# Kernel tuning notes

Measured on AMD Instinct MI355X. Metric: run time of the kernel, lower is better.

Reference implementation:

```python
import jax, jax.numpy as jnp
import numpy as np

VERY_NEGATIVE_NUMBER = -1e30


def setup_inputs() -> dict:
    key = jax.random.key(0)
    ks = jax.random.split(key, 7)
    B, N, M, D = 16, 1024, 1024, 128
    inv_sqrt_d = 1.0 / np.sqrt(D).astype(np.float32)
    query = jax.random.normal(ks[0], (B, N, D), jnp.float32)
    memory = jax.random.normal(ks[1], (B, M, D), jnp.float32)
    # trilinear similarity parameters (BiDAF)
    w_q = jax.random.normal(ks[2], (D,), jnp.float32) * inv_sqrt_d
    w_m = jax.random.normal(ks[3], (D,), jnp.float32) * inv_sqrt_d
    w_qm = jax.random.normal(ks[4], (D,), jnp.float32) * inv_sqrt_d
    query_mask = jax.random.randint(ks[5], (B, N), 0, 2, jnp.int32)
    memory_mask = jax.random.randint(ks[6], (B, M), 0, 2, jnp.int32)
    return {
        "query": query,
        "memory": memory,
        "w_q": w_q,
        "w_m": w_m,
        "w_qm": w_qm,
        "query_mask": query_mask,
        "memory_mask": memory_mask,
    }


def reference(query, memory, w_q, w_m, w_qm, query_mask, memory_mask):
    # trilinear similarity: sim[b,n,m] = w_q.q_n + w_m.m_m + sum_d w_qm_d * q_nd * m_md
    sim = (
        jnp.einsum("bnd,d->bn", query, w_q)[:, :, None]
        + jnp.einsum("bmd,d->bm", memory, w_m)[:, None, :]
        + jnp.einsum("bnd,d,bmd->bnm", query, w_qm, memory)
    )  # [B, N, M]
    mask = (
        query_mask[:, :, None].astype(sim.dtype)
        * memory_mask[:, None, :].astype(sim.dtype)
    )  # [B, N, M]
    sim = sim + (1.0 - mask) * VERY_NEGATIVE_NUMBER
    # query -> memory attention (row-wise softmax over memory axis)
    q2m_prob = jax.nn.softmax(sim, axis=-1)  # [B, N, M]
    query_memory_attention = jnp.einsum("bnm,bmd->bnd", q2m_prob, memory)
    # memory -> query attention (softmax over row maxima, one vector per batch)
    m2q_prob = jax.nn.softmax(jnp.max(sim, axis=-1), axis=-1)  # [B, N]
    m2q = jnp.einsum("bn,bnd->bd", m2q_prob, query)[:, None, :]  # [B, 1, D]
    memory_query_attention = jnp.broadcast_to(m2q, query_memory_attention.shape)
    return (query_memory_attention, memory_query_attention)
```

## Files before the change

### kernel.cpp

```cpp
#include <hip/hip_runtime.h>
#include <hip/hip_bf16.h>
#include <stdint.h>

#define BB 16
#define NN 1024
#define MM 1024
#define DD 128
#define VERY_NEG (-1e30f)
#define LOG2E 1.44269504f
#define NCH 8

using bf16x8 = __attribute__((ext_vector_type(8))) short;
using f32x4  = __attribute__((ext_vector_type(4))) float;

__device__ inline unsigned short f2bf(float f) {
    union { float f; uint32_t u; } cv; cv.f = f;
    uint32_t u = cv.u;
    return (unsigned short)((u + 0x7FFFu + ((u >> 16) & 1u)) >> 16);
}
__device__ inline float bf2f(unsigned short s) {
    union { uint32_t u; float f; } cv; cv.u = ((uint32_t)s) << 16;
    return cv.f;
}
#define EXP2F(x) __builtin_amdgcn_exp2f(x)

typedef __attribute__((address_space(3))) unsigned int lds_u32;
typedef const __attribute__((address_space(1))) unsigned int glb_u32;
__device__ __forceinline__ void gl16(const void* g, void* l) {
    __builtin_amdgcn_global_load_lds((glb_u32*)g, (lds_u32*)l, 16, 0, 0);
}

__global__ __launch_bounds__(256) void prep_all(
    const float* __restrict__ q, const float* __restrict__ mem,
    const float* __restrict__ wq, const float* __restrict__ wm,
    const float* __restrict__ wqm, const int* __restrict__ mmask,
    float* __restrict__ a, float* __restrict__ c1s,
    unsigned short* __restrict__ qp, unsigned short* __restrict__ mb,
    unsigned short* __restrict__ mt)
{
    __shared__ unsigned short t[64][72];
    if (blockIdx.x < 8192) {
        int wave = (blockIdx.x * 256 + threadIdx.x) >> 6;
        int lane = threadIdx.x & 63;
        bool is_q = wave < BB * NN;
        int row = is_q ? wave : wave - BB * NN;
        const float* src = (is_q ? q : mem) + (size_t)row * DD;
        const float* wd  = is_q ? wq : wm;
        float2 v  = *(const float2*)(src + lane * 2);
        float2 w2 = *(const float2*)(wd + lane * 2);
        float dot = v.x * w2.x + v.y * w2.y;
        #pragma unroll
        for (int o = 32; o; o >>= 1) dot += __shfl_xor(dot, o);
        if (lane == 0) {
            if (is_q) a[row] = dot;
            else {
                int mm = mmask[row];
                c1s[row] = (dot + (mm ? 0.f : VERY_NEG)) * LOG2E;
            }
        }
        float2 s2 = v;
        if (is_q) {
            float2 wv = *(const float2*)(wqm + lane * 2);
            s2.x *= wv.x * LOG2E; s2.y *= wv.y * LOG2E;
        }
        ushort2 o2; o2.x = f2bf(s2.x); o2.y = f2bf(s2.y);
        *(ushort2*)((is_q ? qp : mb) + (size_t)row * DD + lane * 2) = o2;
    } else {
        int bid = blockIdx.x - 8192;
        int dt = bid & 1, mtile = (bid >> 1) & 15, b = bid >> 5;
        int d0 = dt * 64, m0 = mtile * 64;
        int tid = threadIdx.x;
        int cc = tid & 63, rr = tid >> 6;
        #pragma unroll
        for (int r = 0; r < 64; r += 4) {
            float v = mem[((size_t)b * MM + m0 + r + rr) * DD + d0 + cc];
            t[cc][r + rr] = f2bf(v);
        }
        __syncthreads();
        #pragma unroll
        for (int r = 0; r < 64; r += 4) {
            mt[((size_t)b * DD + d0 + r + rr) * MM + m0 + cc] = t[r + rr][cc];
        }
    }
}

__global__ __launch_bounds__(256) void flash_fwd(
    const unsigned short* __restrict__ qp, const unsigned short* __restrict__ mb,
    const unsigned short* __restrict__ mt,
    const float* __restrict__ c1s, const int* __restrict__ qmask,
    unsigned short* __restrict__ Opart, float2* __restrict__ ml)
{
    __shared__ unsigned short stg[2][16 * 512];
    __shared__ unsigned short pl[4][2][16][40];
    __shared__ float c1L[256];

    int tid = threadIdx.x;
    int w = tid >> 6, lane = tid & 63;
    int g = lane >> 4, qi = lane & 15;
    int wk = (blockIdx.x & 7) * 64 + (blockIdx.x >> 3);
    int b = wk >> 5, mh = (wk >> 3) & 3, nt = wk & 7;
    int n0q = nt * 128 + w * 32;
    int mbase = mh * 256;

    const unsigned short* mbB = mb + (size_t)b * MM * DD;
    const unsigned short* mtB = mt + (size_t)b * DD * MM;

    if (tid < 64) {
        float4 cv = *(const float4*)(c1s + b * MM + mbase + tid * 4);
        *(float4*)&c1L[tid * 4] = cv;
    }

    const unsigned short* qpb = qp + ((size_t)b * NN + n0q) * DD;
    bf16x8 qf[2][4];
    #pragma unroll
    for (int qt = 0; qt < 2; qt++)
        #pragma unroll
        for (int kc = 0; kc < 4; kc++)
            qf[qt][kc] = *(const bf16x8*)(qpb + (qt * 16 + qi) * DD + kc * 32 + g * 8);

    int qm[2];
    qm[0] = qmask[b * NN + n0q + qi];
    qm[1] = qmask[b * NN + n0q + 16 + qi];

    float m_run[2] = {-INFINITY, -INFINITY}, l_run[2] = {0.f, 0.f};
    f32x4 o[2][8];
    #pragma unroll
    for (int qt = 0; qt < 2; qt++)
        #pragma unroll
        for (int d2 = 0; d2 < 8; d2++) o[qt][d2] = (f32x4){0.f, 0.f, 0.f, 0.f};

    auto stage = [&](int m0, unsigned short* buf) {
        #pragma unroll
        for (int i = 0; i < 4; i++) {
            int j = w * 4 + i;
            if (j < 8) {
                const unsigned short* gsrc = mbB
                    + (size_t)(m0 + (j >> 2) * 16 + (lane & 15)) * DD
                    + (j & 3) * 32 + (lane >> 4) * 8;
                gl16(gsrc, buf + j * 512);
            } else {
                const unsigned short* gsrc = mtB
                    + (size_t)((j - 8) * 16 + (lane & 15)) * MM + m0 + (lane >> 4) * 8;
                gl16(gsrc, buf + j * 512);
            }
        }
    };

    stage(mbase, stg[0]);
    __syncthreads();

    int cur = 0;
    for (int ch = 0; ch < NCH; ch++) {
        int m0 = mbase + ch * 32;
        if (ch + 1 < NCH)
            stage(m0 + 32, stg[cur ^ 1]);

        const unsigned short* bc = stg[cur];

        f32x4 st[2][2];
        #pragma unroll
        for (int qt = 0; qt < 2; qt++) { st[qt][0] = (f32x4){0,0,0,0}; st[qt][1] = (f32x4){0,0,0,0}; }
        #pragma unroll
        for (int t = 0; t < 2; t++) {
            #pragma unroll
            for (int kc = 0; kc < 4; kc++) {
                bf16x8 af = *(const bf16x8*)(bc + ((t * 4 + kc) * 64 + lane) * 8);
                #pragma unroll
                for (int qt = 0; qt < 2; qt++)
                    st[qt][t] = __builtin_amdgcn_mfma_f32_16x16x32_bf16(af, qf[qt][kc], st[qt][t], 0, 0, 0);
            }
        }
        float aL[2][4];
        #pragma unroll
        for (int qt = 0; qt < 2; qt++) {
            float sv[2][4];
            float cmax = -INFINITY;
            #pragma unroll
            for (int t = 0; t < 2; t++) {
                float4 c1v = *(const float4*)&c1L[ch * 32 + t * 16 + g * 4];
                float cc4[4] = {c1v.x, c1v.y, c1v.z, c1v.w};
                #pragma unroll
                for (int i = 0; i < 4; i++) {
                    float s = qm[qt] ? (st[qt][t][i] + cc4[i]) : 0.f;
                    sv[t][i] = s;
                    cmax = fmaxf(cmax, s);
                }
            }
            cmax = fmaxf(cmax, __shfl_xor(cmax, 16));
            cmax = fmaxf(cmax, __shfl_xor(cmax, 32));
            float m_new = fmaxf(m_run[qt], cmax);
            float alpha = EXP2F(m_run[qt] - m_new);
            float psum = 0.f;
            #pragma unroll
            for (int t = 0; t < 2; t++) {
                unsigned short pe[4];
                #pragma unroll
                for (int i = 0; i < 4; i++) {
                    float p = EXP2F(sv[t][i] - m_new);
                    psum += p;
                    pe[i] = f2bf(p);
                }
                ushort4 pw2; pw2.x = pe[0]; pw2.y = pe[1]; pw2.z = pe[2]; pw2.w = pe[3];
                *(ushort4*)(&pl[w][qt][qi][t * 16 + g * 4]) = pw2;
            }
            psum += __shfl_xor(psum, 16);
            psum += __shfl_xor(psum, 32);
            l_run[qt] = l_run[qt] * alpha + psum;
            m_run[qt] = m_new;
            #pragma unroll
            for (int i = 0; i < 4; i++) aL[qt][i] = __shfl(alpha, g * 4 + i);
        }

        __builtin_amdgcn_sched_barrier(0);
        bf16x8 pa[2];
        pa[0] = *(const bf16x8*)(&pl[w][0][qi][g * 8]);
        pa[1] = *(const bf16x8*)(&pl[w][1][qi][g * 8]);
        #pragma unroll
        for (int d2 = 0; d2 < 8; d2++) {
            bf16x8 vf = *(const bf16x8*)(bc + ((8 + d2) * 64 + lane) * 8);
            #pragma unroll
            for (int qt = 0; qt < 2; qt++) {
                f32x4 oo = o[qt][d2];
                #pragma unroll
                for (int i = 0; i < 4; i++) oo[i] *= aL[qt][i];
                o[qt][d2] = __builtin_amdgcn_mfma_f32_16x16x32_bf16(pa[qt], vf, oo, 0, 0, 0);
            }
        }

        __syncthreads();
        cur ^= 1;
    }

    #pragma unroll
    for (int qt = 0; qt < 2; qt++) {
        float inv[4];
        #pragma unroll
        for (int i = 0; i < 4; i++) inv[i] = 1.f / __shfl(l_run[qt], g * 4 + i);
        size_t rbase = ((size_t)mh * BB + b) * NN + n0q + qt * 16;
        #pragma unroll
        for (int d2 = 0; d2 < 8; d2++) {
            #pragma unroll
            for (int i = 0; i < 4; i++)
                Opart[(rbase + g * 4 + i) * DD + d2 * 16 + qi] = f2bf(o[qt][d2][i] * inv[i]);
        }
        if (g == 0) {
            float2 v; v.x = m_run[qt]; v.y = l_run[qt];
            ml[rbase + qi] = v;
        }
    }
}

__global__ __launch_bounds__(256) void merge_kernel(
    const unsigned short* __restrict__ Opart, const float2* __restrict__ ml,
    const float* __restrict__ a, const int* __restrict__ qmask,
    float* __restrict__ out1, float* __restrict__ rowmax)
{
    int R = blockIdx.x * 2 + (threadIdx.x >> 7);
    int d = threadIdx.x & 127;
    float2 mlv[4];
    float M = -INFINITY;
    #pragma unroll
    for (int k = 0; k < 4; k++) {
        mlv[k] = ml[(size_t)k * BB * NN + R];
        M = fmaxf(M, mlv[k].x);
    }
    float wgt[4], Z = 0.f;
    #pragma unroll
    for (int k = 0; k < 4; k++) {
        wgt[k] = mlv[k].y * EXP2F(mlv[k].x - M);
        Z += wgt[k];
    }
    float acc = 0.f;
    #pragma unroll
    for (int k = 0; k < 4; k++)
        acc += bf2f(Opart[((size_t)k * BB * NN + R) * DD + d]) * wgt[k];
    out1[(size_t)R * DD + d] = acc / Z;
    if (d == 0)
        rowmax[R] = M * (1.f / LOG2E) + a[R] + (qmask[R] ? 0.f : VERY_NEG);
}

__global__ __launch_bounds__(256) void m2q_partial(
    const float* __restrict__ rowmax, const float* __restrict__ query,
    float* __restrict__ partial, float* __restrict__ Zbuf)
{
    int bid = blockIdx.x;
    int b = bid >> 4, ch = bid & 15;
    int tid = threadIdx.x, lane = tid & 63, wv = tid >> 6;
    __shared__ float red[8];
    __shared__ float pe[64];
    __shared__ float acc1[128];

    float4 rv = *(const float4*)(rowmax + b * NN + tid * 4);
    float mx = fmaxf(fmaxf(rv.x, rv.y), fmaxf(rv.z, rv.w));
    #pragma unroll
    for (int o = 32; o; o >>= 1) mx = fmaxf(mx, __shfl_xor(mx, o));
    if (lane == 0) red[wv] = mx;
    __syncthreads();
    mx = fmaxf(fmaxf(red[0], red[1]), fmaxf(red[2], red[3]));
    float ls = __expf(rv.x - mx) + __expf(rv.y - mx) + __expf(rv.z - mx) + __expf(rv.w - mx);
    #pragma unroll
    for (int o = 32; o; o >>= 1) ls += __shfl_xor(ls, o);
    if (lane == 0) red[4 + wv] = ls;
    if (tid < 64) pe[tid] = __expf(rowmax[b * NN + ch * 64 + tid] - mx);
    __syncthreads();
    float Z = (red[4] + red[5]) + (red[6] + red[7]);

    int d = tid & 127, h = tid >> 7;
    const float* qb = query + ((size_t)b * NN + ch * 64 + h * 32) * DD + d;
    float acc = 0.f;
    #pragma unroll 8
    for (int n = 0; n < 32; n++) acc += pe[h * 32 + n] * qb[(size_t)n * DD];
    if (h) acc1[d] = acc;
    __syncthreads();
    if (!h) partial[(b * 16 + ch) * DD + d] = acc + acc1[d];
    if (tid == 0) Zbuf[b] = Z;
}

__global__ __launch_bounds__(256) void bcast_kernel(
    const float* __restrict__ partial, const float* __restrict__ Zbuf,
    float4* __restrict__ out2)
{
    __shared__ float m2qL[128];
    int i = blockIdx.x * 256 + threadIdx.x;
    int b = i >> 15;
    int tid = threadIdx.x;
    if (tid < 128) {
        float s = 0.f;
        #pragma unroll
        for (int ch = 0; ch < 16; ch++) s += partial[(b * 16 + ch) * DD + tid];
        m2qL[tid] = s / Zbuf[b];
    }
    __syncthreads();
    out2[i] = ((const float4*)m2qL)[i & 31];
}

extern "C" void kernel_launch(void* const* d_in, const int* in_sizes, int n_in,
                              void* d_out, int out_size, void* d_ws, size_t ws_size,
                              hipStream_t stream)
{
    const float* query  = (const float*)d_in[0];
    const float* memory = (const float*)d_in[1];
    const float* w_q    = (const float*)d_in[2];
    const float* w_m    = (const float*)d_in[3];
    const float* w_qm   = (const float*)d_in[4];
    const int*   qmask  = (const int*)d_in[5];
    const int*   mmask  = (const int*)d_in[6];
    float* out1 = (float*)d_out;
    float* out2 = out1 + (size_t)BB * NN * DD;

    char* ws = (char*)d_ws;
    float* a       = (float*)ws;
    float* c1s     = a + BB * NN;
    float* rowmax  = c1s + BB * MM;
    float* partial = rowmax + BB * NN;
    float* Zbuf    = partial + BB * 16 * DD;
    unsigned short* qp = (unsigned short*)(ws + (1 << 20));
    unsigned short* mb = qp + (size_t)BB * NN * DD;
    unsigned short* mt = mb + (size_t)BB * MM * DD;
    unsigned short* Opart = (unsigned short*)(ws + (16u << 20));
    float2* mlbuf  = (float2*)(ws + (32u << 20));

    prep_all<<<dim3(8192 + 512), 256, 0, stream>>>(query, memory, w_q, w_m, w_qm, mmask,
                                                   a, c1s, qp, mb, mt);
    flash_fwd<<<dim3(512), 256, 0, stream>>>(qp, mb, mt, c1s, qmask, Opart, mlbuf);
    merge_kernel<<<dim3(BB * NN / 2), 256, 0, stream>>>(Opart, mlbuf, a, qmask, out1, rowmax);
    m2q_partial<<<dim3(BB * 16), 256, 0, stream>>>(rowmax, query, partial, Zbuf);
    bcast_kernel<<<dim3(2048), 256, 0, stream>>>(partial, Zbuf, (float4*)out2);
}
```

Before: 57.94 us.

## Switch flash attention to 32x32x16 MFMA with 64-wide chunks and lazy rescaling

```diff
diff --git a/kernel.cpp b/kernel.cpp
--- a/kernel.cpp
+++ b/kernel.cpp
@@ -8,10 +8,12 @@
 #define DD 128
 #define VERY_NEG (-1e30f)
 #define LOG2E 1.44269504f
-#define NCH 8
+#define NCH 4
 
 using bf16x8 = __attribute__((ext_vector_type(8))) short;
 using f32x4  = __attribute__((ext_vector_type(4))) float;
+using f32x16 = __attribute__((ext_vector_type(16))) float;
+using i32x4  = __attribute__((ext_vector_type(4))) int;
 
 __device__ inline unsigned short f2bf(float f) {
     union { float f; uint32_t u; } cv; cv.f = f;
@@ -23,6 +25,12 @@
     return cv.f;
 }
 #define EXP2F(x) __builtin_amdgcn_exp2f(x)
+
+__device__ __forceinline__ int cvtpk(float a, float b) {
+    int r;
+    asm("v_cvt_pk_bf16_f32 %0, %1, %2" : "=v"(r) : "v"(a), "v"(b));
+    return r;
+}
 
 typedef __attribute__((address_space(3))) unsigned int lds_u32;
 typedef const __attribute__((address_space(1))) unsigned int glb_u32;
@@ -90,13 +98,13 @@
     const float* __restrict__ c1s, const int* __restrict__ qmask,
     unsigned short* __restrict__ Opart, float2* __restrict__ ml)
 {
-    __shared__ unsigned short stg[2][16 * 512];
-    __shared__ unsigned short pl[4][2][16][40];
+    __shared__ unsigned short stg[2][32 * 512];
     __shared__ float c1L[256];
 
     int tid = threadIdx.x;
     int w = tid >> 6, lane = tid & 63;
-    int g = lane >> 4, qi = lane & 15;
+    int l31 = lane & 31, hi = lane >> 5, hi4 = hi * 4;
+    bool lo = (lane < 32);
     int wk = (blockIdx.x & 7) * 64 + (blockIdx.x >> 3);
     int b = wk >> 5, mh = (wk >> 3) & 3, nt = wk & 7;
     int n0q = nt * 128 + w * 32;
@@ -111,38 +119,32 @@
     }
 
     const unsigned short* qpb = qp + ((size_t)b * NN + n0q) * DD;
-    bf16x8 qf[2][4];
-    #pragma unroll
-    for (int qt = 0; qt < 2; qt++)
-        #pragma unroll
-        for (int kc = 0; kc < 4; kc++)
-            qf[qt][kc] = *(const bf16x8*)(qpb + (qt * 16 + qi) * DD + kc * 32 + g * 8);
-
-    int qm[2];
-    qm[0] = qmask[b * NN + n0q + qi];
-    qm[1] = qmask[b * NN + n0q + 16 + qi];
-
-    float m_run[2] = {-INFINITY, -INFINITY}, l_run[2] = {0.f, 0.f};
-    f32x4 o[2][8];
-    #pragma unroll
-    for (int qt = 0; qt < 2; qt++)
-        #pragma unroll
-        for (int d2 = 0; d2 < 8; d2++) o[qt][d2] = (f32x4){0.f, 0.f, 0.f, 0.f};
+    bf16x8 qf[8];
+    #pragma unroll
+    for (int dk = 0; dk < 8; dk++)
+        qf[dk] = *(const bf16x8*)(qpb + l31 * DD + dk * 16 + hi * 8);
+
+    int qmv = qmask[b * NN + n0q + l31];
+
+    float m_run = -INFINITY, l_run = 0.f, tmax = -INFINITY;
+    f32x16 o[4];
+    #pragma unroll
+    for (int d0 = 0; d0 < 4; d0++)
+        #pragma unroll
+        for (int r = 0; r < 16; r++) o[d0][r] = 0.f;
 
     auto stage = [&](int m0, unsigned short* buf) {
         #pragma unroll
-        for (int i = 0; i < 4; i++) {
-            int j = w * 4 + i;
-            if (j < 8) {
-                const unsigned short* gsrc = mbB
-                    + (size_t)(m0 + (j >> 2) * 16 + (lane & 15)) * DD
-                    + (j & 3) * 32 + (lane >> 4) * 8;
-                gl16(gsrc, buf + j * 512);
+        for (int i = 0; i < 8; i++) {
+            int s = w * 8 + i;
+            const unsigned short* g;
+            if (s < 16) {
+                g = mbB + (size_t)(m0 + (s >> 3) * 32 + l31) * DD + (s & 7) * 16 + hi * 8;
             } else {
-                const unsigned short* gsrc = mtB
-                    + (size_t)((j - 8) * 16 + (lane & 15)) * MM + m0 + (lane >> 4) * 8;
-                gl16(gsrc, buf + j * 512);
-            }
+                int s2 = s - 16;
+                g = mtB + (size_t)((s2 >> 2) * 32 + l31) * MM + m0 + (s2 & 3) * 16 + hi * 8;
+            }
+            gl16(g, buf + s * 512);
         }
     };
 
@@ -151,102 +153,114 @@
 
     int cur = 0;
     for (int ch = 0; ch < NCH; ch++) {
-        int m0 = mbase + ch * 32;
+        int m0 = mbase + ch * 64;
         if (ch + 1 < NCH)
-            stage(m0 + 32, stg[cur ^ 1]);
+            stage(m0 + 64, stg[cur ^ 1]);
 
         const unsigned short* bc = stg[cur];
 
-        f32x4 st[2][2];
-        #pragma unroll
-        for (int qt = 0; qt < 2; qt++) { st[qt][0] = (f32x4){0,0,0,0}; st[qt][1] = (f32x4){0,0,0,0}; }
-        #pragma unroll
-        for (int t = 0; t < 2; t++) {
-            #pragma unroll
-            for (int kc = 0; kc < 4; kc++) {
-                bf16x8 af = *(const bf16x8*)(bc + ((t * 4 + kc) * 64 + lane) * 8);
-                #pragma unroll
-                for (int qt = 0; qt < 2; qt++)
-                    st[qt][t] = __builtin_amdgcn_mfma_f32_16x16x32_bf16(af, qf[qt][kc], st[qt][t], 0, 0, 0);
-            }
-        }
-        float aL[2][4];
-        #pragma unroll
-        for (int qt = 0; qt < 2; qt++) {
-            float sv[2][4];
-            float cmax = -INFINITY;
-            #pragma unroll
-            for (int t = 0; t < 2; t++) {
-                float4 c1v = *(const float4*)&c1L[ch * 32 + t * 16 + g * 4];
-                float cc4[4] = {c1v.x, c1v.y, c1v.z, c1v.w};
+        f32x16 stt[2];
+        #pragma unroll
+        for (int t = 0; t < 2; t++)
+            #pragma unroll
+            for (int r = 0; r < 16; r++) stt[t][r] = 0.f;
+        #pragma unroll
+        for (int t = 0; t < 2; t++)
+            #pragma unroll
+            for (int dk = 0; dk < 8; dk++) {
+                bf16x8 af = *(const bf16x8*)(bc + (t * 8 + dk) * 512 + lane * 8);
+                stt[t] = __builtin_amdgcn_mfma_f32_32x32x16_bf16(af, qf[dk], stt[t], 0, 0, 0);
+            }
+
+        float sv[2][16];
+        float pmax = -INFINITY;
+        #pragma unroll
+        for (int t = 0; t < 2; t++)
+            #pragma unroll
+            for (int rq = 0; rq < 4; rq++) {
+                float4 c4 = *(const float4*)&c1L[ch * 64 + t * 32 + rq * 8 + hi4];
+                float cc4[4] = {c4.x, c4.y, c4.z, c4.w};
                 #pragma unroll
                 for (int i = 0; i < 4; i++) {
-                    float s = qm[qt] ? (st[qt][t][i] + cc4[i]) : 0.f;
-                    sv[t][i] = s;
-                    cmax = fmaxf(cmax, s);
+                    float s = qmv ? (stt[t][rq * 4 + i] + cc4[i]) : 0.f;
+                    sv[t][rq * 4 + i] = s;
+                    pmax = fmaxf(pmax, s);
                 }
             }
-            cmax = fmaxf(cmax, __shfl_xor(cmax, 16));
-            cmax = fmaxf(cmax, __shfl_xor(cmax, 32));
-            float m_new = fmaxf(m_run[qt], cmax);
-            float alpha = EXP2F(m_run[qt] - m_new);
-            float psum = 0.f;
-            #pragma unroll
-            for (int t = 0; t < 2; t++) {
-                unsigned short pe[4];
-                #pragma unroll
-                for (int i = 0; i < 4; i++) {
-                    float p = EXP2F(sv[t][i] - m_new);
-                    psum += p;
-                    pe[i] = f2bf(p);
-                }
-                ushort4 pw2; pw2.x = pe[0]; pw2.y = pe[1]; pw2.z = pe[2]; pw2.w = pe[3];
-                *(ushort4*)(&pl[w][qt][qi][t * 16 + g * 4]) = pw2;
-            }
-            psum += __shfl_xor(psum, 16);
-            psum += __shfl_xor(psum, 32);
-            l_run[qt] = l_run[qt] * alpha + psum;
-            m_run[qt] = m_new;
-            #pragma unroll
-            for (int i = 0; i < 4; i++) aL[qt][i] = __shfl(alpha, g * 4 + i);
-        }
-
-        __builtin_amdgcn_sched_barrier(0);
-        bf16x8 pa[2];
-        pa[0] = *(const bf16x8*)(&pl[w][0][qi][g * 8]);
-        pa[1] = *(const bf16x8*)(&pl[w][1][qi][g * 8]);
-        #pragma unroll
-        for (int d2 = 0; d2 < 8; d2++) {
-            bf16x8 vf = *(const bf16x8*)(bc + ((8 + d2) * 64 + lane) * 8);
-            #pragma unroll
-            for (int qt = 0; qt < 2; qt++) {
-                f32x4 oo = o[qt][d2];
-                #pragma unroll
-                for (int i = 0; i < 4; i++) oo[i] *= aL[qt][i];
-                o[qt][d2] = __builtin_amdgcn_mfma_f32_16x16x32_bf16(pa[qt], vf, oo, 0, 0, 0);
-            }
+        pmax = fmaxf(pmax, __shfl_xor(pmax, 32));
+        tmax = fmaxf(tmax, pmax);
+
+        if (__any(pmax > m_run + 8.f)) {
+            float m_new = fmaxf(m_run, pmax);
+            float alphaL = EXP2F(m_run - m_new);
+            m_run = m_new;
+            l_run *= alphaL;
+            #pragma unroll
+            for (int rg = 0; rg < 16; rg++) {
+                float ar = __shfl(alphaL, ((rg & 3) + 8 * (rg >> 2)) + hi4);
+                o[0][rg] *= ar; o[1][rg] *= ar; o[2][rg] *= ar; o[3][rg] *= ar;
+            }
+        }
+
+        float psum = 0.f;
+        bf16x8 pfrag[4];
+        #pragma unroll
+        for (int t = 0; t < 2; t++) {
+            float p[16];
+            #pragma unroll
+            for (int r = 0; r < 16; r++) {
+                p[r] = EXP2F(sv[t][r] - m_run);
+                psum += p[r];
+            }
+            #pragma unroll
+            for (int h = 0; h < 2; h++) {
+                int A0 = cvtpk(p[h * 8 + 0], p[h * 8 + 1]);
+                int A1 = cvtpk(p[h * 8 + 2], p[h * 8 + 3]);
+                int B0 = cvtpk(p[h * 8 + 4], p[h * 8 + 5]);
+                int B1 = cvtpk(p[h * 8 + 6], p[h * 8 + 7]);
+                int xA0 = __shfl_xor(A0, 32), xA1 = __shfl_xor(A1, 32);
+                int xB0 = __shfl_xor(B0, 32), xB1 = __shfl_xor(B1, 32);
+                i32x4 fw;
+                fw[0] = lo ? A0 : xB0;
+                fw[1] = lo ? A1 : xB1;
+                fw[2] = lo ? xA0 : B0;
+                fw[3] = lo ? xA1 : B1;
+                pfrag[t * 2 + h] = __builtin_bit_cast(bf16x8, fw);
+            }
+        }
+        psum += __shfl_xor(psum, 32);
+        l_run += psum;
+
+        #pragma unroll
+        for (int d0 = 0; d0 < 4; d0++) {
+            f32x16 oo = o[d0];
+            #pragma unroll
+            for (int k4 = 0; k4 < 4; k4++) {
+                bf16x8 vf = *(const bf16x8*)(bc + (16 + d0 * 4 + k4) * 512 + lane * 8);
+                oo = __builtin_amdgcn_mfma_f32_32x32x16_bf16(pfrag[k4], vf, oo, 0, 0, 0);
+            }
+            o[d0] = oo;
         }
 
         __syncthreads();
         cur ^= 1;
     }
 
-    #pragma unroll
-    for (int qt = 0; qt < 2; qt++) {
-        float inv[4];
-        #pragma unroll
-        for (int i = 0; i < 4; i++) inv[i] = 1.f / __shfl(l_run[qt], g * 4 + i);
-        size_t rbase = ((size_t)mh * BB + b) * NN + n0q + qt * 16;
-        #pragma unroll
-        for (int d2 = 0; d2 < 8; d2++) {
-            #pragma unroll
-            for (int i = 0; i < 4; i++)
-                Opart[(rbase + g * 4 + i) * DD + d2 * 16 + qi] = f2bf(o[qt][d2][i] * inv[i]);
-        }
-        if (g == 0) {
-            float2 v; v.x = m_run[qt]; v.y = l_run[qt];
-            ml[rbase + qi] = v;
-        }
+    float invL = 1.f / l_run;
+    size_t rbase = ((size_t)mh * BB + b) * NN + n0q;
+    #pragma unroll
+    for (int rg = 0; rg < 16; rg++) {
+        float ir = __shfl(invL, ((rg & 3) + 8 * (rg >> 2)) + hi4);
+        int qv = (rg & 3) + 8 * (rg >> 2) + hi4;
+        size_t rowb = (rbase + qv) * DD + l31;
+        Opart[rowb + 0 * 32] = f2bf(o[0][rg] * ir);
+        Opart[rowb + 1 * 32] = f2bf(o[1][rg] * ir);
+        Opart[rowb + 2 * 32] = f2bf(o[2][rg] * ir);
+        Opart[rowb + 3 * 32] = f2bf(o[3][rg] * ir);
+    }
+    if (lo) {
+        float2 v; v.x = tmax; v.y = l_run * EXP2F(m_run - tmax);
+        ml[rbase + l31] = v;
     }
 }
 
```

After: 64.39 us. 11.1% more time.

## Split memory axis into more chunks when workspace allows, add MFMA priority hints

Applied to the files above, without the earlier changes.

```diff
diff --git a/kernel.cpp b/kernel.cpp
--- a/kernel.cpp
+++ b/kernel.cpp
@@ -8,7 +8,6 @@
 #define DD 128
 #define VERY_NEG (-1e30f)
 #define LOG2E 1.44269504f
-#define NCH 8
 
 using bf16x8 = __attribute__((ext_vector_type(8))) short;
 using f32x4  = __attribute__((ext_vector_type(4))) float;
@@ -88,7 +87,8 @@
     const unsigned short* __restrict__ qp, const unsigned short* __restrict__ mb,
     const unsigned short* __restrict__ mt,
     const float* __restrict__ c1s, const int* __restrict__ qmask,
-    unsigned short* __restrict__ Opart, float2* __restrict__ ml)
+    unsigned short* __restrict__ Opart, float2* __restrict__ ml,
+    int mspan, int nch, int mh_bits, int MHC)
 {
     __shared__ unsigned short stg[2][16 * 512];
     __shared__ unsigned short pl[4][2][16][40];
@@ -97,15 +97,18 @@
     int tid = threadIdx.x;
     int w = tid >> 6, lane = tid & 63;
     int g = lane >> 4, qi = lane & 15;
-    int wk = (blockIdx.x & 7) * 64 + (blockIdx.x >> 3);
-    int b = wk >> 5, mh = (wk >> 3) & 3, nt = wk & 7;
+    int cpx = gridDim.x >> 3;
+    int wk = (blockIdx.x & 7) * cpx + (blockIdx.x >> 3);
+    int b = wk >> (3 + mh_bits);
+    int mh = (wk >> 3) & (MHC - 1);
+    int nt = wk & 7;
     int n0q = nt * 128 + w * 32;
-    int mbase = mh * 256;
+    int mbase = mh * mspan;
 
     const unsigned short* mbB = mb + (size_t)b * MM * DD;
     const unsigned short* mtB = mt + (size_t)b * DD * MM;
 
-    if (tid < 64) {
+    if (tid * 4 < mspan) {
         float4 cv = *(const float4*)(c1s + b * MM + mbase + tid * 4);
         *(float4*)&c1L[tid * 4] = cv;
     }
@@ -150,9 +153,9 @@
     __syncthreads();
 
     int cur = 0;
-    for (int ch = 0; ch < NCH; ch++) {
+    for (int ch = 0; ch < nch; ch++) {
         int m0 = mbase + ch * 32;
-        if (ch + 1 < NCH)
+        if (ch + 1 < nch)
             stage(m0 + 32, stg[cur ^ 1]);
 
         const unsigned short* bc = stg[cur];
@@ -160,6 +163,7 @@
         f32x4 st[2][2];
         #pragma unroll
         for (int qt = 0; qt < 2; qt++) { st[qt][0] = (f32x4){0,0,0,0}; st[qt][1] = (f32x4){0,0,0,0}; }
+        __builtin_amdgcn_s_setprio(1);
         #pragma unroll
         for (int t = 0; t < 2; t++) {
             #pragma unroll
@@ -170,6 +174,7 @@
                     st[qt][t] = __builtin_amdgcn_mfma_f32_16x16x32_bf16(af, qf[qt][kc], st[qt][t], 0, 0, 0);
             }
         }
+        __builtin_amdgcn_s_setprio(0);
         float aL[2][4];
         #pragma unroll
         for (int qt = 0; qt < 2; qt++) {
@@ -215,6 +220,7 @@
         bf16x8 pa[2];
         pa[0] = *(const bf16x8*)(&pl[w][0][qi][g * 8]);
         pa[1] = *(const bf16x8*)(&pl[w][1][qi][g * 8]);
+        __builtin_amdgcn_s_setprio(1);
         #pragma unroll
         for (int d2 = 0; d2 < 8; d2++) {
             bf16x8 vf = *(const bf16x8*)(bc + ((8 + d2) * 64 + lane) * 8);
@@ -226,6 +232,7 @@
                 o[qt][d2] = __builtin_amdgcn_mfma_f32_16x16x32_bf16(pa[qt], vf, oo, 0, 0, 0);
             }
         }
+        __builtin_amdgcn_s_setprio(0);
 
         __syncthreads();
         cur ^= 1;
@@ -253,27 +260,20 @@
 __global__ __launch_bounds__(256) void merge_kernel(
     const unsigned short* __restrict__ Opart, const float2* __restrict__ ml,
     const float* __restrict__ a, const int* __restrict__ qmask,
-    float* __restrict__ out1, float* __restrict__ rowmax)
+    float* __restrict__ out1, float* __restrict__ rowmax, int MHC)
 {
     int R = blockIdx.x * 2 + (threadIdx.x >> 7);
     int d = threadIdx.x & 127;
-    float2 mlv[4];
     float M = -INFINITY;
-    #pragma unroll
-    for (int k = 0; k < 4; k++) {
-        mlv[k] = ml[(size_t)k * BB * NN + R];
-        M = fmaxf(M, mlv[k].x);
-    }
-    float wgt[4], Z = 0.f;
-    #pragma unroll
-    for (int k = 0; k < 4; k++) {
-        wgt[k] = mlv[k].y * EXP2F(mlv[k].x - M);
-        Z += wgt[k];
-    }
-    float acc = 0.f;
-    #pragma unroll
-    for (int k = 0; k < 4; k++)
-        acc += bf2f(Opart[((size_t)k * BB * NN + R) * DD + d]) * wgt[k];
+    for (int k = 0; k < MHC; k++)
+        M = fmaxf(M, ml[(size_t)k * BB * NN + R].x);
+    float Z = 0.f, acc = 0.f;
+    for (int k = 0; k < MHC; k++) {
+        float2 v = ml[(size_t)k * BB * NN + R];
+        float wgt = v.y * EXP2F(v.x - M);
+        Z += wgt;
+        acc += bf2f(Opart[((size_t)k * BB * NN + R) * DD + d]) * wgt;
+    }
     out1[(size_t)R * DD + d] = acc / Z;
     if (d == 0)
         rowmax[R] = M * (1.f / LOG2E) + a[R] + (qmask[R] ? 0.f : VERY_NEG);
@@ -357,13 +357,18 @@
     unsigned short* qp = (unsigned short*)(ws + (1 << 20));
     unsigned short* mb = qp + (size_t)BB * NN * DD;
     unsigned short* mt = mb + (size_t)BB * MM * DD;
-    unsigned short* Opart = (unsigned short*)(ws + (16u << 20));
-    float2* mlbuf  = (float2*)(ws + (32u << 20));
+
+    size_t need8 = ((size_t)13 << 20) + (size_t)8 * BB * NN * DD * 2 + (size_t)8 * BB * NN * 8;
+    int MHC = (ws_size >= need8) ? 8 : 4;
+    int mspan = MM / MHC, nch = mspan / 32, mh_bits = (MHC == 8) ? 3 : 2;
+    unsigned short* Opart = (unsigned short*)(ws + (13u << 20));
+    float2* mlbuf = (float2*)(ws + (13u << 20) + (size_t)MHC * BB * NN * DD * 2);
 
     prep_all<<<dim3(8192 + 512), 256, 0, stream>>>(query, memory, w_q, w_m, w_qm, mmask,
                                                    a, c1s, qp, mb, mt);
-    flash_fwd<<<dim3(512), 256, 0, stream>>>(qp, mb, mt, c1s, qmask, Opart, mlbuf);
-    merge_kernel<<<dim3(BB * NN / 2), 256, 0, stream>>>(Opart, mlbuf, a, qmask, out1, rowmax);
+    flash_fwd<<<dim3(128 * MHC), 256, 0, stream>>>(qp, mb, mt, c1s, qmask, Opart, mlbuf,
+                                                   mspan, nch, mh_bits, MHC);
+    merge_kernel<<<dim3(BB * NN / 2), 256, 0, stream>>>(Opart, mlbuf, a, qmask, out1, rowmax, MHC);
     m2q_partial<<<dim3(BB * 16), 256, 0, stream>>>(rowmax, query, partial, Zbuf);
     bcast_kernel<<<dim3(2048), 256, 0, stream>>>(partial, Zbuf, (float4*)out2);
 }
```

Result: slower. 75.61 us (+30.5%).
